# Kernel tuning notes

Measured on AMD Instinct MI355X. Metric: run time of the kernel, lower is better.

## Reference

```python
import jax, jax.numpy as jnp
import numpy as np

NA = 4096
NB = 4096
MAX_ITER = 20

def setup_inputs() -> dict:
    key = jax.random.key(0)
    k1, k2, k3 = jax.random.split(key, 3)
    AT = jax.random.uniform(k1, (NA,), dtype=jnp.float32)
    BT = jax.random.uniform(k2, (NB,), dtype=jnp.float32)
    param = jax.random.uniform(k3, (NA, NB), dtype=jnp.float32)
    return {"AT": AT, "BT": BT, "param": param}

def _solve(AT, BT, K):
    # fixed-point iteration: AF = AT/(1+K@BF), BF = BT/(1+K^T@AF)
    def body(carry, _):
        AF, BF = carry
        AF = AT / (1.0 + K @ BF)
        BF = BT / (1.0 + AF @ K)
        return (AF, BF), None
    (AF, BF), _ = jax.lax.scan(body, (AT, BT), None, length=MAX_ITER)
    return AF, BF

def reference(AT, BT, param):
    K = jnp.square(param)              # reparameterize='square'
    AF, BF = _solve(AT, BT, K)
    # one more iterate (the 'last_iterate' pass) producing the output C
    AF = AT / (1.0 + K @ BF)
    BF = BT / (1.0 + AF @ K)
    C = K * AF[:, None] * BF[None, :]  # [nA, nB]
    return C
```

## Files before the change

### kernel.cpp

```cpp
#include <hip/hip_runtime.h>


constexpr int N     = 4096;
constexpr int NITER = 21;
constexpr int NBLK  = 256;
constexpr int RREG  = 7;
constexpr int RLDS  = 16 - RREG;

__device__ __forceinline__ float ld_agent(const float* p) {
    return __hip_atomic_load(p, __ATOMIC_RELAXED, __HIP_MEMORY_SCOPE_AGENT);
}
__device__ __forceinline__ void st_agent(float* p, float v) {
    __hip_atomic_store(p, v, __ATOMIC_RELAXED, __HIP_MEMORY_SCOPE_AGENT);
}
__device__ __forceinline__ void sync_lds() {
    asm volatile("s_waitcnt lgkmcnt(0)" ::: "memory");
    __builtin_amdgcn_s_barrier();
    asm volatile("" ::: "memory");
}

__device__ __forceinline__ float poll_sum16(const float* p, float sgn) {
    float v[16];
    #pragma unroll
    for (int g = 0; g < 16; ++g) v[g] = ld_agent(p + (size_t)g * N);
    for (;;) {
        bool ok = true;
        #pragma unroll
        for (int g = 0; g < 16; ++g) {
            if (!(v[g] * sgn > 1e-9f)) { ok = false; v[g] = ld_agent(p + (size_t)g * N); }
        }
        if (ok) break;
    }
    float s = 0.0f;
    #pragma unroll
    for (int g = 0; g < 16; ++g) s += v[g];
    return s * sgn;
}

__global__ void
__attribute__((amdgpu_flat_work_group_size(256, 256)))
__attribute__((amdgpu_waves_per_eu(1, 1)))
competitive_persistent(const float* __restrict__ AT, const float* __restrict__ BT,
                       const float* __restrict__ P,  float* __restrict__ C,
                       float* __restrict__ ws)
{
    const int b  = blockIdx.x;
    const int t  = threadIdx.x;
    const int bR = b >> 4, bC = b & 15;
    const int R0 = bR << 8, C0 = bC << 8;
    const int rl = t >> 4, cl = t & 15;
    const int row0 = R0 + rl * 16;
    const int col0 = C0 + cl * 16;
    const int w    = t >> 6;

    float* yrp = ws;
    float* ycp = ws + 3 * 16 * (size_t)N;

    __shared__ __align__(16) float xsh[256];
    __shared__ __align__(16) float xsh2[256];
    __shared__ __align__(16) float red[1024];
    __shared__ __align__(16) float kl[16][RLDS][256];

    float k[RREG * 16];
    #pragma unroll
    for (int r = 0; r < 16; ++r) {
        const float4* src = (const float4*)(P + (size_t)(row0 + r) * N + col0);
        #pragma unroll
        for (int q = 0; q < 4; ++q) {
            float4 v = src[q];
            float4 s;
            s.x = v.x * v.x; s.y = v.y * v.y; s.z = v.z * v.z; s.w = v.w * v.w;
            if (r < RREG) {
                k[r * 16 + q * 4 + 0] = s.x;
                k[r * 16 + q * 4 + 1] = s.y;
                k[r * 16 + q * 4 + 2] = s.z;
                k[r * 16 + q * 4 + 3] = s.w;
            } else {
                *(float4*)&kl[rl][r - RREG][cl * 16 + q * 4] = s;
            }
        }
    }
    sync_lds();

    #pragma unroll 1
    for (int it = 0; it < NITER; ++it) {
        const int   sC      = it % 3;
        const float sgn_cur = (it & 1) ? -1.0f : 1.0f;

        if (it > 0) {
            const int sP = (it + 2) % 3;
            const float sum = poll_sum16(ycp + (size_t)sP * 16 * N + C0 + t, -sgn_cur);
            xsh[t] = BT[C0 + t] / (1.0f + sum);
        } else {
            xsh[t] = BT[C0 + t];
        }
        sync_lds();

        {
            float xv[16];
            const float4* xs4 = (const float4*)(xsh + cl * 16);
            #pragma unroll
            for (int q = 0; q < 4; ++q) {
                float4 v = xs4[q];
                xv[q * 4 + 0] = v.x; xv[q * 4 + 1] = v.y;
                xv[q * 4 + 2] = v.z; xv[q * 4 + 3] = v.w;
            }
            float part[16];
            #pragma unroll
            for (int r = 0; r < 16; ++r) part[r] = 0.0f;
            #pragma unroll
            for (int c = 0; c < 16; ++c) {
                const float x = xv[c];
                #pragma unroll
                for (int r = 0; r < RREG; ++r)
                    part[r] = fmaf(k[r * 16 + c], x, part[r]);
            }
            #pragma unroll
            for (int r = RREG; r < 16; ++r) {
                const float4* kp = (const float4*)&kl[rl][r - RREG][cl * 16];
                #pragma unroll
                for (int q = 0; q < 4; ++q) {
                    float4 kv = kp[q];
                    part[r] = fmaf(kv.x, xv[q * 4 + 0], part[r]);
                    part[r] = fmaf(kv.y, xv[q * 4 + 1], part[r]);
                    part[r] = fmaf(kv.z, xv[q * 4 + 2], part[r]);
                    part[r] = fmaf(kv.w, xv[q * 4 + 3], part[r]);
                }
            }
            #pragma unroll
            for (int off = 1; off < 16; off <<= 1) {
                #pragma unroll
                for (int r = 0; r < 16; ++r)
                    part[r] += __shfl_xor(part[r], off, 64);
            }
            float myv = part[0];
            #pragma unroll
            for (int r = 1; r < 16; ++r) myv = (cl == r) ? part[r] : myv;
            st_agent(yrp + ((size_t)sC * 16 + bC) * N + R0 + t, sgn_cur * myv);
        }

        {
            const float sum = poll_sum16(yrp + (size_t)sC * 16 * N + R0 + t, sgn_cur);
            xsh2[t] = AT[R0 + t] / (1.0f + sum);
        }
        sync_lds();

        {
            float av[16];
            #pragma unroll
            for (int r = 0; r < 16; ++r) av[r] = xsh2[rl * 16 + r];
            float part[16];
            #pragma unroll
            for (int c = 0; c < 16; ++c) part[c] = 0.0f;
            #pragma unroll
            for (int r = 0; r < RREG; ++r) {
                const float a = av[r];
                #pragma unroll
                for (int c = 0; c < 16; ++c)
                    part[c] = fmaf(k[r * 16 + c], a, part[c]);
            }
            #pragma unroll
            for (int r = RREG; r < 16; ++r) {
                const float a = av[r];
                const float4* kp = (const float4*)&kl[rl][r - RREG][cl * 16];
                #pragma unroll
                for (int q = 0; q < 4; ++q) {
                    float4 kv = kp[q];
                    part[q * 4 + 0] = fmaf(kv.x, a, part[q * 4 + 0]);
                    part[q * 4 + 1] = fmaf(kv.y, a, part[q * 4 + 1]);
                    part[q * 4 + 2] = fmaf(kv.z, a, part[q * 4 + 2]);
                    part[q * 4 + 3] = fmaf(kv.w, a, part[q * 4 + 3]);
                }
            }
            #pragma unroll
            for (int c = 0; c < 16; ++c) {
                part[c] += __shfl_xor(part[c], 16, 64);
                part[c] += __shfl_xor(part[c], 32, 64);
            }
            if ((t & 63) < 16) {
                #pragma unroll
                for (int c = 0; c < 16; ++c)
                    red[w * 256 + cl * 16 + c] = part[c];
            }
            sync_lds();
            const float s4 = red[t] + red[256 + t] + red[512 + t] + red[768 + t];
            st_agent(ycp + ((size_t)sC * 16 + bR) * N + C0 + t, sgn_cur * s4);
        }
    }

    sync_lds();
    {
        const float sum = poll_sum16(ycp + (size_t)2 * 16 * N + C0 + t, 1.0f);
        red[t] = BT[C0 + t] / (1.0f + sum);
    }
    sync_lds();

    float af[16], bf[16];
    #pragma unroll
    for (int r = 0; r < 16; ++r) af[r] = xsh2[rl * 16 + r];
    #pragma unroll
    for (int c = 0; c < 16; ++c) bf[c] = red[cl * 16 + c];

    #pragma unroll
    for (int r = 0; r < 16; ++r) {
        float4* dst = (float4*)(C + (size_t)(row0 + r) * N + col0);
        const float a = af[r];
        #pragma unroll
        for (int q = 0; q < 4; ++q) {
            float4 kv;
            if (r < RREG) {
                kv.x = k[r * 16 + q * 4 + 0];
                kv.y = k[r * 16 + q * 4 + 1];
                kv.z = k[r * 16 + q * 4 + 2];
                kv.w = k[r * 16 + q * 4 + 3];
            } else {
                kv = *(const float4*)&kl[rl][r - RREG][cl * 16 + q * 4];
            }
            float4 o;
            o.x = kv.x * a * bf[q * 4 + 0];
            o.y = kv.y * a * bf[q * 4 + 1];
            o.z = kv.z * a * bf[q * 4 + 2];
            o.w = kv.w * a * bf[q * 4 + 3];
            dst[q] = o;
        }
    }
}

extern "C" void kernel_launch(void* const* d_in, const int* in_sizes, int n_in,
                              void* d_out, int out_size, void* d_ws, size_t ws_size,
                              hipStream_t stream) {
    const float* AT = (const float*)d_in[0];
    const float* BT = (const float*)d_in[1];
    const float* P  = (const float*)d_in[2];
    float*       C  = (float*)d_out;
    float*       ws = (float*)d_ws;

    hipMemsetAsync(d_ws, 0, 2 * 3 * 16 * (size_t)N * sizeof(float), stream);

    competitive_persistent<<<dim3(NBLK), dim3(256), 0, stream>>>(AT, BT, P, C, ws);
}
```

Before: 303.7 us.

## Transpose partial-sum workspace so each poll reads one 64-byte line

The workspace of partial sums is transposed so the 16 partials for one output element are contiguous. Each poll is then four dwordx4 loads with sc0 sc1 cache bypass in inline asm, instead of 16 scattered strided atomic loads, and backs off with s_sleep. The LDS copy of K is re-laid out so each lane's float4 reads are lane-contiguous, avoiding bank conflicts. The cost is that every poll retry now re-reads the whole line, and the stores from 16 producer blocks scatter into shared lines.

```diff
diff --git a/kernel.cpp b/kernel.cpp
--- a/kernel.cpp
+++ b/kernel.cpp
@@ -7,6 +7,8 @@
 constexpr int RREG  = 7;
 constexpr int RLDS  = 16 - RREG;
 
+typedef float f32x4 __attribute__((ext_vector_type(4)));
+
 __device__ __forceinline__ float ld_agent(const float* p) {
     return __hip_atomic_load(p, __ATOMIC_RELAXED, __HIP_MEMORY_SCOPE_AGENT);
 }
@@ -19,22 +21,35 @@
     asm volatile("" ::: "memory");
 }
 
-__device__ __forceinline__ float poll_sum16(const float* p, float sgn) {
-    float v[16];
-    #pragma unroll
-    for (int g = 0; g < 16; ++g) v[g] = ld_agent(p + (size_t)g * N);
+__device__ __forceinline__ float poll_line16(const float* p, float sgn) {
     for (;;) {
+        f32x4 a, b, c, d;
+        asm volatile(
+            "global_load_dwordx4 %0, %4, off sc0 sc1\n\t"
+            "global_load_dwordx4 %1, %4, off offset:16 sc0 sc1\n\t"
+            "global_load_dwordx4 %2, %4, off offset:32 sc0 sc1\n\t"
+            "global_load_dwordx4 %3, %4, off offset:48 sc0 sc1\n\t"
+            "s_waitcnt vmcnt(0)"
+            : "=&v"(a), "=&v"(b), "=&v"(c), "=&v"(d)
+            : "v"(p)
+            : "memory");
         bool ok = true;
         #pragma unroll
-        for (int g = 0; g < 16; ++g) {
-            if (!(v[g] * sgn > 1e-9f)) { ok = false; v[g] = ld_agent(p + (size_t)g * N); }
-        }
-        if (ok) break;
-    }
-    float s = 0.0f;
-    #pragma unroll
-    for (int g = 0; g < 16; ++g) s += v[g];
-    return s * sgn;
+        for (int i = 0; i < 4; ++i) {
+            ok &= (a[i] * sgn > 1e-9f);
+            ok &= (b[i] * sgn > 1e-9f);
+            ok &= (c[i] * sgn > 1e-9f);
+            ok &= (d[i] * sgn > 1e-9f);
+        }
+        if (ok) {
+            float s = ((a[0] + a[1]) + (a[2] + a[3]))
+                    + ((b[0] + b[1]) + (b[2] + b[3]))
+                    + ((c[0] + c[1]) + (c[2] + c[3]))
+                    + ((d[0] + d[1]) + (d[2] + d[3]));
+            return s * sgn;
+        }
+        __builtin_amdgcn_s_sleep(1);
+    }
 }
 
 __global__ void
@@ -52,14 +67,15 @@
     const int row0 = R0 + rl * 16;
     const int col0 = C0 + cl * 16;
     const int w    = t >> 6;
+    const int l    = t & 63;
 
     float* yrp = ws;
-    float* ycp = ws + 3 * 16 * (size_t)N;
+    float* ycp = ws + 3 * (size_t)N * 16;
 
     __shared__ __align__(16) float xsh[256];
     __shared__ __align__(16) float xsh2[256];
     __shared__ __align__(16) float red[1024];
-    __shared__ __align__(16) float kl[16][RLDS][256];
+    __shared__ __align__(16) f32x4 kl4[RLDS * 4 * 4 * 64];
 
     float k[RREG * 16];
     #pragma unroll
@@ -68,15 +84,16 @@
         #pragma unroll
         for (int q = 0; q < 4; ++q) {
             float4 v = src[q];
-            float4 s;
-            s.x = v.x * v.x; s.y = v.y * v.y; s.z = v.z * v.z; s.w = v.w * v.w;
             if (r < RREG) {
-                k[r * 16 + q * 4 + 0] = s.x;
-                k[r * 16 + q * 4 + 1] = s.y;
-                k[r * 16 + q * 4 + 2] = s.z;
-                k[r * 16 + q * 4 + 3] = s.w;
+                k[r * 16 + q * 4 + 0] = v.x * v.x;
+                k[r * 16 + q * 4 + 1] = v.y * v.y;
+                k[r * 16 + q * 4 + 2] = v.z * v.z;
+                k[r * 16 + q * 4 + 3] = v.w * v.w;
             } else {
-                *(float4*)&kl[rl][r - RREG][cl * 16 + q * 4] = s;
+                f32x4 s;
+                s[0] = v.x * v.x; s[1] = v.y * v.y;
+                s[2] = v.z * v.z; s[3] = v.w * v.w;
+                kl4[(((r - RREG) * 4 + q) * 4 + w) * 64 + l] = s;
             }
         }
     }
@@ -89,7 +106,8 @@
 
         if (it > 0) {
             const int sP = (it + 2) % 3;
-            const float sum = poll_sum16(ycp + (size_t)sP * 16 * N + C0 + t, -sgn_cur);
+            const float sum =
+                poll_line16(ycp + ((size_t)sP * N + C0 + t) * 16, -sgn_cur);
             xsh[t] = BT[C0 + t] / (1.0f + sum);
         } else {
             xsh[t] = BT[C0 + t];
@@ -117,14 +135,13 @@
             }
             #pragma unroll
             for (int r = RREG; r < 16; ++r) {
-                const float4* kp = (const float4*)&kl[rl][r - RREG][cl * 16];
                 #pragma unroll
                 for (int q = 0; q < 4; ++q) {
-                    float4 kv = kp[q];
-                    part[r] = fmaf(kv.x, xv[q * 4 + 0], part[r]);
-                    part[r] = fmaf(kv.y, xv[q * 4 + 1], part[r]);
-                    part[r] = fmaf(kv.z, xv[q * 4 + 2], part[r]);
-                    part[r] = fmaf(kv.w, xv[q * 4 + 3], part[r]);
+                    f32x4 kv = kl4[(((r - RREG) * 4 + q) * 4 + w) * 64 + l];
+                    part[r] = fmaf(kv[0], xv[q * 4 + 0], part[r]);
+                    part[r] = fmaf(kv[1], xv[q * 4 + 1], part[r]);
+                    part[r] = fmaf(kv[2], xv[q * 4 + 2], part[r]);
+                    part[r] = fmaf(kv[3], xv[q * 4 + 3], part[r]);
                 }
             }
             #pragma unroll
@@ -136,11 +153,12 @@
             float myv = part[0];
             #pragma unroll
             for (int r = 1; r < 16; ++r) myv = (cl == r) ? part[r] : myv;
-            st_agent(yrp + ((size_t)sC * 16 + bC) * N + R0 + t, sgn_cur * myv);
+            st_agent(yrp + ((size_t)sC * N + R0 + t) * 16 + bC, sgn_cur * myv);
         }
 
         {
-            const float sum = poll_sum16(yrp + (size_t)sC * 16 * N + R0 + t, sgn_cur);
+            const float sum =
+                poll_line16(yrp + ((size_t)sC * N + R0 + t) * 16, sgn_cur);
             xsh2[t] = AT[R0 + t] / (1.0f + sum);
         }
         sync_lds();
@@ -162,14 +180,13 @@
             #pragma unroll
             for (int r = RREG; r < 16; ++r) {
                 const float a = av[r];
-                const float4* kp = (const float4*)&kl[rl][r - RREG][cl * 16];
                 #pragma unroll
                 for (int q = 0; q < 4; ++q) {
-                    float4 kv = kp[q];
-                    part[q * 4 + 0] = fmaf(kv.x, a, part[q * 4 + 0]);
-                    part[q * 4 + 1] = fmaf(kv.y, a, part[q * 4 + 1]);
-                    part[q * 4 + 2] = fmaf(kv.z, a, part[q * 4 + 2]);
-                    part[q * 4 + 3] = fmaf(kv.w, a, part[q * 4 + 3]);
+                    f32x4 kv = kl4[(((r - RREG) * 4 + q) * 4 + w) * 64 + l];
+                    part[q * 4 + 0] = fmaf(kv[0], a, part[q * 4 + 0]);
+                    part[q * 4 + 1] = fmaf(kv[1], a, part[q * 4 + 1]);
+                    part[q * 4 + 2] = fmaf(kv[2], a, part[q * 4 + 2]);
+                    part[q * 4 + 3] = fmaf(kv[3], a, part[q * 4 + 3]);
                 }
             }
             #pragma unroll
@@ -184,13 +201,13 @@
             }
             sync_lds();
             const float s4 = red[t] + red[256 + t] + red[512 + t] + red[768 + t];
-            st_agent(ycp + ((size_t)sC * 16 + bR) * N + C0 + t, sgn_cur * s4);
+            st_agent(ycp + ((size_t)sC * N + C0 + t) * 16 + bR, sgn_cur * s4);
         }
     }
 
     sync_lds();
     {
-        const float sum = poll_sum16(ycp + (size_t)2 * 16 * N + C0 + t, 1.0f);
+        const float sum = poll_line16(ycp + ((size_t)2 * N + C0 + t) * 16, 1.0f);
         red[t] = BT[C0 + t] / (1.0f + sum);
     }
     sync_lds();
@@ -207,20 +224,20 @@
         const float a = af[r];
         #pragma unroll
         for (int q = 0; q < 4; ++q) {
-            float4 kv;
+            f32x4 kv;
             if (r < RREG) {
-                kv.x = k[r * 16 + q * 4 + 0];
-                kv.y = k[r * 16 + q * 4 + 1];
-                kv.z = k[r * 16 + q * 4 + 2];
-                kv.w = k[r * 16 + q * 4 + 3];
+                kv[0] = k[r * 16 + q * 4 + 0];
+                kv[1] = k[r * 16 + q * 4 + 1];
+                kv[2] = k[r * 16 + q * 4 + 2];
+                kv[3] = k[r * 16 + q * 4 + 3];
             } else {
-                kv = *(const float4*)&kl[rl][r - RREG][cl * 16 + q * 4];
+                kv = kl4[(((r - RREG) * 4 + q) * 4 + w) * 64 + l];
             }
             float4 o;
-            o.x = kv.x * a * bf[q * 4 + 0];
-            o.y = kv.y * a * bf[q * 4 + 1];
-            o.z = kv.z * a * bf[q * 4 + 2];
-            o.w = kv.w * a * bf[q * 4 + 3];
+            o.x = kv[0] * a * bf[q * 4 + 0];
+            o.y = kv[1] * a * bf[q * 4 + 1];
+            o.z = kv[2] * a * bf[q * 4 + 2];
+            o.w = kv[3] * a * bf[q * 4 + 3];
             dst[q] = o;
         }
     }
@@ -235,7 +252,7 @@
     float*       C  = (float*)d_out;
     float*       ws = (float*)d_ws;
 
-    hipMemsetAsync(d_ws, 0, 2 * 3 * 16 * (size_t)N * sizeof(float), stream);
+    hipMemsetAsync(d_ws, 0, 2 * 3 * (size_t)N * 16 * sizeof(float), stream);
 
     competitive_persistent<<<dim3(NBLK), dim3(256), 0, stream>>>(AT, BT, P, C, ws);
 }
```

Measured after the change: 474.9 us. +56.3%, slower.
